# Kernel optimization log

Measured on AMD Instinct MI355X. Metric: run time of the kernel, lower is better.

The kernel has to match this reference:

```python
import jax, jax.numpy as jnp
import numpy as np

G = 384          # voxel grid extent per axis = (15.36*2)/0.08
HALF = G // 2
SZ = G
SYZ = G * G
SXYZ = G * G * G
VOX = 0.08       # layer voxel size (cfg voxel_size * coord_key)
CK = 2           # coord_key / tensor stride
K = 5            # grid conv kernel size -> 125 offsets
GN = 7           # grid_num -> 343 cells per ROI, pooling conv kernel
EPS = 1e-5


def _masked_bn(x, valid, gamma, beta):
    # training-mode batch norm over valid rows only
    v = valid[:, None].astype(x.dtype)
    n = jnp.maximum(v.sum(), 1.0)
    mean = (x * v).sum(0) / n
    var = (((x - mean) ** 2) * v).sum(0) / n
    return (x - mean) * jax.lax.rsqrt(var + EPS) * gamma + beta


def setup_inputs() -> dict:
    rng = np.random.default_rng(0)
    B, R, C = 4, 128, 128
    P = GN ** 3
    N = B * R * P           # 175616 grid points
    Nv = 200000             # active voxels in sp_tensor
    # unique sparse-tensor coordinates: sample linear codes, dedupe, decode
    codes = np.unique(rng.integers(0, B * SXYZ, size=3 * Nv))[:Nv]
    rng.shuffle(codes)
    sb = codes // SXYZ
    rem = codes % SXYZ
    vx, vy, vz = rem // SYZ, (rem % SYZ) // SZ, rem % SZ
    sp_coords = np.stack(
        [sb, (vx - HALF) * CK, (vy - HALF) * CK, (vz - HALF) * CK], 1
    ).astype(np.int32)
    # ROI grid points: dense (7,7,7) grids inside random boxes
    centers = rng.uniform(-12.0, 12.0, (B, R, 3)).astype(np.float32)
    sizes = rng.uniform(0.5, 3.0, (B, R, 3)).astype(np.float32)
    gi = np.stack(
        np.meshgrid(np.arange(GN), np.arange(GN), np.arange(GN), indexing='ij'), -1
    ).reshape(-1, 3).astype(np.float32)  # [343,3]
    pts = (centers[:, :, None, :] - sizes[:, :, None, :] / 2
           + (gi[None, None] + 0.5) / GN * sizes[:, :, None, :])  # [B,R,P,3]
    bcol = np.broadcast_to(np.arange(B, dtype=np.float32)[:, None, None, None], (B, R, P, 1))
    grid_points = np.concatenate([bcol, pts], -1).reshape(N, 4)
    k1, k2, k3 = jax.random.split(jax.random.key(0), 3)
    return {
        'sp_coords': jnp.asarray(sp_coords),
        'sp_feats': jax.random.normal(k1, (Nv, C), jnp.float32),
        'grid_points': jnp.asarray(grid_points),
        'W1': jax.random.normal(k2, (K ** 3, C, C), jnp.float32) * 0.01,
        'gamma1': jnp.ones((C,), jnp.float32),
        'beta1': jnp.zeros((C,), jnp.float32),
        'W2': jax.random.normal(k3, (P, C, C), jnp.float32) * 0.01,
        'gamma2': jnp.ones((C,), jnp.float32),
        'beta2': jnp.zeros((C,), jnp.float32),
    }


def reference(sp_coords, sp_feats, grid_points, W1, gamma1, beta1, W2, gamma2, beta2):
    N = grid_points.shape[0]
    C = sp_feats.shape[1]
    P = GN ** 3
    # --- voxelize grid points and merge coordinates (hash) ---
    vox = jnp.clip(jnp.floor(grid_points[:, 1:4] / VOX).astype(jnp.int32),
                   -(HALF - 1), HALF - 1)
    pos = vox + HALF
    bidx = grid_points[:, 0].astype(jnp.int32)
    mc = bidx * SXYZ + pos[:, 0] * SYZ + pos[:, 1] * SZ + pos[:, 2]
    unq, unq_inv = jnp.unique(mc, return_inverse=True, size=N, fill_value=-1)
    valid = unq >= 0
    u = jnp.maximum(unq, 0)
    qb = u // SXYZ
    qv = jnp.stack([u % SXYZ // SYZ, u % SYZ // SZ, u % SZ], 1)  # voxel idx [Nq,3]
    # --- hash table for sp_tensor coords (sorted linear codes) ---
    svi = sp_coords[:, 1:4] // CK + HALF
    scode = sp_coords[:, 0] * SXYZ + svi[:, 0] * SYZ + svi[:, 1] * SZ + svi[:, 2]
    order = jnp.argsort(scode)
    scodes = scode[order]
    sfeats = sp_feats[order]
    # --- Minkowski-style sparse conv: sum over 125 kernel offsets ---
    kr = jnp.arange(-(K // 2), K // 2 + 1)
    offs = jnp.stack(jnp.meshgrid(kr, kr, kr, indexing='ij'), -1).reshape(-1, 3)

    def body(acc, xs):
        off, Wk = xs
        tvi = qv + off
        inb = jnp.all((tvi >= 0) & (tvi < G), axis=1) & valid
        code = qb * SXYZ + tvi[:, 0] * SYZ + tvi[:, 1] * SZ + tvi[:, 2]
        p = jnp.clip(jnp.searchsorted(scodes, code), 0, scodes.shape[0] - 1)
        hit = (scodes[p] == code) & inb
        f = jnp.where(hit[:, None], sfeats[p], 0.0)
        return acc + f @ Wk, None

    acc, _ = jax.lax.scan(body, jnp.zeros((N, C), sp_feats.dtype), (offs, W1))
    x = jax.nn.elu(_masked_bn(acc, valid, gamma1, beta1))
    # gather back per grid point, then dense pooling conv over full 7^3 grid
    nf = x[unq_inv].reshape(-1, P, C)              # [num_rois, 343, C]
    pooled = jnp.einsum('bpc,pcd->bd', nf, W2)     # pooling conv at center
    mean = pooled.mean(0)
    var = pooled.var(0)
    return (pooled - mean) * jax.lax.rsqrt(var + EPS) * gamma2 + beta2
```

## Files before the change

kernel.cpp:

```cpp
#include <hip/hip_runtime.h>
#include <math.h>

#define GG     384
#define HALFG  192
#define SZc    384
#define SYZc   147456
#define SXYZc  56623104
#define CC     128
#define PP     343
#define KK     125
#define TBSLOTS (1 << 20)
#define TBMASK  (TBSLOTS - 1)
#define BMAXc   4
#define NCOL    (BMAXc * GG * GG)
#define TASLOTS (1 << 19)
#define TAMASK  (TASLOTS - 1)
#define CAPK   2048
#define CAPP   1024
#define EPSc   1e-5f
#define PAD    16

typedef unsigned long long u64;

__device__ __forceinline__ unsigned hash32(int code) {
    unsigned h = (unsigned)code;
    h ^= h >> 16; h *= 0x7feb352du;
    h ^= h >> 15; h *= 0x846ca68bu;
    h ^= h >> 16;
    return h;
}

__global__ void k_buildInsert(const float* __restrict__ gp, int2* tabA, int* slotA,
                              int* nq, int* ucode, int N, int nbA,
                              const int4* __restrict__ spc4, unsigned* tabB,
                              u64* colBM, int Nv) {
    if (blockIdx.x < nbA) {
        __shared__ int lcnt, lbase;
        if (threadIdx.x == 0) lcnt = 0;
        __syncthreads();
        int i = blockIdx.x * 256 + threadIdx.x;
        int myloc = -1; unsigned myh = 0; int code = 0;
        if (i < N) {
            float4 g = ((const float4*)gp)[i];
            int b = (int)g.x;
            int vx = (int)floorf(g.y / 0.08f); vx = min(max(vx, -(HALFG - 1)), HALFG - 1);
            int vy = (int)floorf(g.z / 0.08f); vy = min(max(vy, -(HALFG - 1)), HALFG - 1);
            int vz = (int)floorf(g.w / 0.08f); vz = min(max(vz, -(HALFG - 1)), HALFG - 1);
            code = b * SXYZc + (vx + HALFG) * SYZc + (vy + HALFG) * SZc + (vz + HALFG);
            unsigned h = hash32(code) & TAMASK;
            while (true) {
                int old = atomicCAS(&tabA[h].x, 0, code + 1);
                if (old == 0) { myloc = atomicAdd(&lcnt, 1); break; }
                if (old == code + 1) break;
                h = (h + 1) & TAMASK;
            }
            myh = h;
            slotA[i] = (int)h;
        }
        __syncthreads();
        if (threadIdx.x == 0 && lcnt > 0) lbase = atomicAdd(nq, lcnt);
        __syncthreads();
        if (myloc >= 0) {
            int uid = lbase + myloc;
            tabA[myh].y = uid;
            ucode[uid] = code;
        }
    } else {
        int i = (blockIdx.x - nbA) * 256 + threadIdx.x;
        if (i >= Nv) return;
        int4 s = spc4[i];
        int b = s.x;
        int x = (s.y >> 1) + HALFG;
        int y = (s.z >> 1) + HALFG;
        int z = (s.w >> 1) + HALFG;
        int code = b * SXYZc + x * SYZc + y * SZc + z;
        unsigned h = hash32(code);
        unsigned slot = h & TBMASK;
        unsigned val = ((h >> 18) << 18) | (unsigned)(i + 1);
        while (true) {
            unsigned old = atomicCAS(&tabB[slot], 0u, val);
            if (old == 0u) break;
            slot = (slot + 1) & TBMASK;
        }
        int col = (b * GG + x) * GG + y;
        atomicOr(&colBM[(size_t)col * 6 + (z >> 6)], 1ull << (z & 63));
    }
}

__global__ void k_probe(const int* __restrict__ ucode, const u64* __restrict__ colBM,
                        const unsigned* __restrict__ tabB, const int4* __restrict__ spc4,
                        int* hmark, int* cntk, int* bkUid, int* bkP,
                        const int* __restrict__ nqp, int N) {
    unsigned tid = blockIdx.x * 256u + threadIdx.x;
    if (tid >= (unsigned)N * 25u) return;
    unsigned uid = tid / 25u;
    if (uid >= (unsigned)(*nqp)) return;
    int c = (int)(tid - uid * 25u);
    unsigned code = (unsigned)ucode[uid];
    unsigned b = code / SXYZc; unsigned rem = code - b * SXYZc;
    int x = (int)(rem / SYZc); rem -= (unsigned)x * SYZc;
    int y = (int)(rem / SZc);
    int z = (int)(rem - (unsigned)y * SZc);
    int dx = c / 5, dy = c - dx * 5;
    int cx = x + dx - 2, cy = y + dy - 2;
    if ((unsigned)cx >= GG || (unsigned)cy >= GG) return;
    const u64* bm = colBM + (size_t)(((int)b * GG + cx) * GG + cy) * 6;
    int lo = max(z - 2, 0);
    int hi = min(z + 2, GG - 1);
    int width = hi - lo + 1;
    int i0 = lo >> 6, sh = lo & 63;
    u64 w = bm[i0] >> sh;
    if (sh + width > 64) w |= bm[i0 + 1] << (64 - sh);
    unsigned bits = (unsigned)(w & ((1ull << width) - 1ull));
    if (bits == 0) return;
    hmark[uid] = 1;
    int zbase = z - 2;
    while (bits) {
        int j = __builtin_ctz(bits);
        bits &= bits - 1;
        int tz = lo + j;
        int dz = tz - zbase;
        int k = c * 5 + dz;
        int tcode = (int)b * SXYZc + cx * SYZc + cy * SZc + tz;
        unsigned h = hash32(tcode);
        unsigned slot = h & TBMASK;
        unsigned tag = h >> 18;
        while (true) {
            unsigned v = tabB[slot];
            if (v == 0u) break;
            if ((v >> 18) == tag) {
                int row = (int)(v & 0x3FFFFu) - 1;
                int4 s = spc4[row];
                int rcode = s.x * SXYZc + ((s.y >> 1) + HALFG) * SYZc
                          + ((s.z >> 1) + HALFG) * SZc + ((s.w >> 1) + HALFG);
                if (rcode == tcode) {
                    int pos = atomicAdd(&cntk[k * PAD], 1);
                    if (pos < CAPK) { bkUid[k * CAPK + pos] = (int)uid; bkP[k * CAPK + pos] = row; }
                    break;
                }
            }
            slot = (slot + 1) & TBMASK;
        }
    }
}

__global__ void k_hitPairs(const int* __restrict__ hmark, int* hitList, int* nh,
                           float* acc, const int* __restrict__ nqp, int nbU,
                           const int* __restrict__ slotA, const int2* __restrict__ tabA,
                           int* pcnt, int* pairPack, int N) {
    if (blockIdx.x < nbU) {
        __shared__ int lcnt, lbase;
        if (threadIdx.x == 0) lcnt = 0;
        __syncthreads();
        int i = blockIdx.x * 256 + threadIdx.x;
        int myloc = -1;
        if (i < *nqp && hmark[i]) myloc = atomicAdd(&lcnt, 1);
        __syncthreads();
        if (threadIdx.x == 0 && lcnt > 0) lbase = atomicAdd(nh, lcnt);
        __syncthreads();
        if (myloc >= 0) {
            hitList[lbase + myloc] = i;
            float4* a4 = (float4*)(acc + (size_t)i * CC);
            float4 z4 = make_float4(0.f, 0.f, 0.f, 0.f);
            #pragma unroll
            for (int c = 0; c < CC / 4; c++) a4[c] = z4;
        }
    } else {
        int i = (blockIdx.x - nbU) * 256 + threadIdx.x;
        if (i >= N) return;
        int uid = tabA[slotA[i]].y;
        if (!hmark[uid]) return;
        int b = i / PP;
        int p = i - b * PP;
        int pos = atomicAdd(&pcnt[p * PAD], 1);
        if (pos < CAPP) pairPack[p * CAPP + pos] = (b << 18) | uid;
    }
}

__global__ __launch_bounds__(256) void k_conv(const float* __restrict__ spf,
        const float* __restrict__ W1, const int* __restrict__ cntk,
        const int* __restrict__ bkUid, const int* __restrict__ bkP, float* acc) {
    int k = blockIdx.x;
    int cob = blockIdx.y * 64;
    int t = threadIdx.x;
    int co = cob + (t & 63);
    int lane = t >> 6;
    int cnt = min(cntk[k * PAD], CAPK);
    __shared__ float fs[32][CC];
    __shared__ int hrS[32];
    const float* Wk = W1 + (size_t)k * CC * CC;
    for (int tile = blockIdx.z * 32; tile < cnt; tile += 32 * gridDim.z) {
        int nt = min(32, cnt - tile);
        if (t < nt) hrS[t] = bkUid[k * CAPK + tile + t];
        for (int e = t; e < 32 * CC; e += 256) {
            int r = e >> 7, cc = e & 127;
            fs[r][cc] = (r < nt) ? spf[(size_t)bkP[k * CAPK + tile + r] * CC + cc] : 0.f;
        }
        __syncthreads();
        float a[8] = {0.f, 0.f, 0.f, 0.f, 0.f, 0.f, 0.f, 0.f};
        for (int ci = 0; ci < CC; ci++) {
            float wv = Wk[(size_t)ci * CC + co];
            #pragma unroll
            for (int j = 0; j < 8; j++) a[j] += fs[lane * 8 + j][ci] * wv;
        }
        #pragma unroll
        for (int j = 0; j < 8; j++) {
            int r = lane * 8 + j;
            if (r < nt) atomicAdd(&acc[(size_t)hrS[r] * CC + co], a[j]);
        }
        __syncthreads();
    }
}

__global__ void k_stats(const float* __restrict__ acc, const int* __restrict__ hitList,
                        float* gsum, float* gsumsq, const int* __restrict__ nhp,
                        int* done, const float* __restrict__ g1, const float* __restrict__ b1,
                        float* scaleV, float* shiftV, float* c0v, const int* __restrict__ nqp) {
    int t = threadIdx.x; int c = t & 127; int half = t >> 7;
    int nh = *nhp;
    float s = 0.f, s2 = 0.f;
    for (int j = blockIdx.x * 2 + half; j < nh; j += gridDim.x * 2) {
        int r = hitList[j];
        float v = acc[(size_t)r * CC + c];
        s += v; s2 += v * v;
    }
    __shared__ float red[256];
    red[t] = s; __syncthreads();
    if (half == 0) atomicAdd(&gsum[c * PAD], s + red[t + 128]);
    __syncthreads();
    red[t] = s2; __syncthreads();
    if (half == 0) atomicAdd(&gsumsq[c * PAD], s2 + red[t + 128]);
    __syncthreads();
    __shared__ int lastS;
    if (t == 0) {
        __threadfence();
        lastS = (atomicAdd(done, 1) == gridDim.x - 1) ? 1 : 0;
    }
    __syncthreads();
    if (lastS && t < 128) {
        float n = (float)max(*nqp, 1);
        float sum  = atomicAdd(&gsum[t * PAD], 0.f);
        float sums = atomicAdd(&gsumsq[t * PAD], 0.f);
        float mean = sum / n;
        float var = sums / n - mean * mean;
        float rs = 1.0f / sqrtf(var + EPSc);
        float scale = rs * g1[t];
        float shift = b1[t] - mean * scale;
        float c0 = shift;
        c0 = c0 > 0.f ? c0 : expm1f(c0);
        scaleV[t] = scale; shiftV[t] = shift; c0v[t] = c0;
    }
}

__global__ __launch_bounds__(256) void k_pool(const float* __restrict__ acc,
        const float* __restrict__ W2, const int* __restrict__ pcnt,
        const int* __restrict__ pairPack,
        const float* __restrict__ scaleV, const float* __restrict__ shiftV,
        const float* __restrict__ c0v, float* pooled) {
    int p = blockIdx.x;
    int cob = blockIdx.y * 64;
    int t = threadIdx.x;
    int co = cob + (t & 63);
    int lane = t >> 6;
    int cnt = min(pcnt[p * PAD], CAPP);
    __shared__ float fs[32][CC];
    __shared__ int bS[32];
    __shared__ float scS[CC], shS[CC], c0S[CC];
    if (t < 128) { scS[t] = scaleV[t]; shS[t] = shiftV[t]; c0S[t] = c0v[t]; }
    __syncthreads();
    const float* Wp = W2 + (size_t)p * CC * CC;
    for (int tile = blockIdx.z * 32; tile < cnt; tile += 32 * gridDim.z) {
        int nt = min(32, cnt - tile);
        if (t < nt) bS[t] = pairPack[p * CAPP + tile + t] >> 18;
        for (int e = t; e < 32 * CC; e += 256) {
            int r = e >> 7, cc = e & 127;
            float v = 0.f;
            if (r < nt) {
                int uid = pairPack[p * CAPP + tile + r] & 0x3FFFF;
                float x = acc[(size_t)uid * CC + cc] * scS[cc] + shS[cc];
                x = x > 0.f ? x : expm1f(x);
                v = x - c0S[cc];
            }
            fs[r][cc] = v;
        }
        __syncthreads();
        float a[8] = {0.f, 0.f, 0.f, 0.f, 0.f, 0.f, 0.f, 0.f};
        for (int ci = 0; ci < CC; ci++) {
            float wv = Wp[(size_t)ci * CC + co];
            #pragma unroll
            for (int j = 0; j < 8; j++) a[j] += fs[lane * 8 + j][ci] * wv;
        }
        #pragma unroll
        for (int j = 0; j < 8; j++) {
            int r = lane * 8 + j;
            if (r < nt) atomicAdd(&pooled[(size_t)bS[r] * CC + co], a[j]);
        }
        __syncthreads();
    }
}

__global__ void k_bn2(const float* __restrict__ pooled, const float* __restrict__ g2,
                      const float* __restrict__ b2, float* out, int NB) {
    int d = blockIdx.x; int t = threadIdx.x;
    float s = 0.f;
    for (int b = t; b < NB; b += 64) s += pooled[(size_t)b * CC + d];
    for (int o = 32; o >= 1; o >>= 1) s += __shfl_xor(s, o, 64);
    float mean = s / (float)NB;
    float s2 = 0.f;
    for (int b = t; b < NB; b += 64) { float v = pooled[(size_t)b * CC + d] - mean; s2 += v * v; }
    for (int o = 32; o >= 1; o >>= 1) s2 += __shfl_xor(s2, o, 64);
    float rs = 1.0f / sqrtf(s2 / (float)NB + EPSc);
    float gg = g2[d], bb = b2[d];
    for (int b = t; b < NB; b += 64)
        out[(size_t)b * CC + d] = (pooled[(size_t)b * CC + d] - mean) * rs * gg + bb;
}

extern "C" void kernel_launch(void* const* d_in, const int* in_sizes, int n_in,
                              void* d_out, int out_size, void* d_ws, size_t ws_size,
                              hipStream_t stream) {
    (void)n_in; (void)out_size; (void)ws_size;
    const int*   spc = (const int*)d_in[0];
    const float* spf = (const float*)d_in[1];
    const float* gp  = (const float*)d_in[2];
    const float* W1  = (const float*)d_in[3];
    const float* g1  = (const float*)d_in[4];
    const float* b1  = (const float*)d_in[5];
    const float* W2  = (const float*)d_in[6];
    const float* g2  = (const float*)d_in[7];
    const float* b2  = (const float*)d_in[8];
    int Nv = in_sizes[0] / 4;
    int N  = in_sizes[2] / 4;
    int NB = N / PP;
    float* out = (float*)d_out;

    char* w = (char*)d_ws;
    char* zero0 = w;
    int* nq   = (int*)w;  int* nh = nq + 1;  int* done = nq + 2;  w += 64;
    unsigned* tabB = (unsigned*)w; w += (size_t)TBSLOTS * 4;
    int2*     tabA = (int2*)w;     w += (size_t)TASLOTS * 8;
    u64* colBM = (u64*)w;         w += (size_t)NCOL * 6 * 8;
    int* cntk = (int*)w;          w += 128 * PAD * 4;
    int* pcnt = (int*)w;          w += 344 * PAD * 4;
    float* gsum   = (float*)w;    w += 128 * PAD * 4;
    float* gsumsq = (float*)w;    w += 128 * PAD * 4;
    int* hmark    = (int*)w;      w += (size_t)N * 4;
    float* pooled = (float*)w;    w += (size_t)NB * CC * 4;
    size_t zbytes = (size_t)(w - zero0);
    float* scaleV = (float*)w;    w += 128 * 4;
    float* shiftV = (float*)w;    w += 128 * 4;
    float* c0v    = (float*)w;    w += 128 * 4;
    int* hitList = (int*)w;       w += (size_t)N * 4;
    int* ucode   = (int*)w;       w += (size_t)N * 4;
    int* slotA   = (int*)w;       w += (size_t)N * 4;
    int* bkUid   = (int*)w;       w += (size_t)KK * CAPK * 4;
    int* bkP     = (int*)w;       w += (size_t)KK * CAPK * 4;
    int* pairPack= (int*)w;       w += (size_t)PP * CAPP * 4;
    float* acc   = (float*)w;     w += (size_t)N * CC * 4;

    hipMemsetAsync(zero0, 0, zbytes, stream);

    int nbA = (N + 255) / 256;
    int nbB = (Nv + 255) / 256;
    k_buildInsert<<<nbA + nbB, 256, 0, stream>>>(gp, tabA, slotA, nq, ucode, N, nbA,
                                                 (const int4*)spc, tabB, colBM, Nv);
    long tot = (long)N * 25;
    k_probe  <<<(unsigned)((tot + 255) / 256), 256, 0, stream>>>(ucode, colBM, tabB,
                                                                 (const int4*)spc,
                                                                 hmark, cntk, bkUid, bkP, nq, N);
    int nbU = (N + 255) / 256;
    k_hitPairs<<<nbU + nbA, 256, 0, stream>>>(hmark, hitList, nh, acc, nq, nbU,
                                              slotA, tabA, pcnt, pairPack, N);
    k_conv   <<<dim3(KK, 2, 4), 256, 0, stream>>>(spf, W1, cntk, bkUid, bkP, acc);
    k_stats  <<<256, 256, 0, stream>>>(acc, hitList, gsum, gsumsq, nh, done,
                                       g1, b1, scaleV, shiftV, c0v, nq);
    k_pool   <<<dim3(PP, 2, 2), 256, 0, stream>>>(acc, W2, pcnt, pairPack,
                                                  scaleV, shiftV, c0v, pooled);
    k_bn2    <<<CC, 64, 0, stream>>>(pooled, g2, b2, out, NB);
}
```

Baseline: 350.2 us.

## Fuse whole pipeline into one cooperative persistent kernel with grid syncs

Replaces the memset and seven separate kernel launches with a single cooperative persistent kernel. Stages are separated by grid-wide barriers, and the in-kernel zeroing of the workspace replaces hipMemsetAsync. The goal is to remove per-launch overhead and the tail idle time between small dependent stages. The trade-offs are grid-stride loops in place of natural grid shapes, possibly lower occupancy for the heavy conv and pool stages, and the cost of the grid.sync barriers themselves.

```diff
diff --git a/kernel.cpp b/kernel.cpp
--- a/kernel.cpp
+++ b/kernel.cpp
@@ -1,5 +1,8 @@
 #include <hip/hip_runtime.h>
+#include <hip/hip_cooperative_groups.h>
 #include <math.h>
+
+namespace cg = cooperative_groups;
 
 #define GG     384
 #define HALFG  192
@@ -30,18 +33,44 @@
     return h;
 }
 
-__global__ void k_buildInsert(const float* __restrict__ gp, int2* tabA, int* slotA,
-                              int* nq, int* ucode, int N, int nbA,
-                              const int4* __restrict__ spc4, unsigned* tabB,
-                              u64* colBM, int Nv) {
-    if (blockIdx.x < nbA) {
-        __shared__ int lcnt, lbase;
-        if (threadIdx.x == 0) lcnt = 0;
-        __syncthreads();
-        int i = blockIdx.x * 256 + threadIdx.x;
+struct Prm {
+    const float* gp; const int4* spc4; const float* spf;
+    const float* W1; const float* g1; const float* b1;
+    const float* W2; const float* g2; const float* b2;
+    float* out;
+    int2* tabA; unsigned* tabB; u64* colBM;
+    int* slotA; int* ucode; int* nq; int* nh;
+    int* hmark; int* hitList; int* cntk; int* pcnt;
+    int* bkUid; int* bkP; int* pairPack;
+    float* gsum; float* gsumsq; float* acc; float* pooled;
+    float4* zero0; size_t z16; int N; int Nv; int NB;
+};
+
+__global__ __launch_bounds__(256, 4) void k_fused(Prm p) {
+    cg::grid_group grid = cg::this_grid();
+    const int nb = (int)gridDim.x;
+    const int bid = blockIdx.x, t = threadIdx.x;
+
+    __shared__ float fs[32][CC];
+    __shared__ int idxS[32];
+    __shared__ float scS[CC], shS[CC], c0S[CC];
+    __shared__ float red[256];
+    __shared__ int lcnt, lbase;
+
+    {
+        float4 z4 = make_float4(0.f, 0.f, 0.f, 0.f);
+        for (size_t e = (size_t)bid * 256 + t; e < p.z16; e += (size_t)nb * 256)
+            p.zero0[e] = z4;
+    }
+    grid.sync();
+
+    for (int base = bid * 256; base < p.N; base += nb * 256) {
+        if (t == 0) lcnt = 0;
+        __syncthreads();
+        int i = base + t;
         int myloc = -1; unsigned myh = 0; int code = 0;
-        if (i < N) {
-            float4 g = ((const float4*)gp)[i];
+        if (i < p.N) {
+            float4 g = ((const float4*)p.gp)[i];
             int b = (int)g.x;
             int vx = (int)floorf(g.y / 0.08f); vx = min(max(vx, -(HALFG - 1)), HALFG - 1);
             int vy = (int)floorf(g.z / 0.08f); vy = min(max(vy, -(HALFG - 1)), HALFG - 1);
@@ -49,26 +78,26 @@
             code = b * SXYZc + (vx + HALFG) * SYZc + (vy + HALFG) * SZc + (vz + HALFG);
             unsigned h = hash32(code) & TAMASK;
             while (true) {
-                int old = atomicCAS(&tabA[h].x, 0, code + 1);
+                int old = atomicCAS(&p.tabA[h].x, 0, code + 1);
                 if (old == 0) { myloc = atomicAdd(&lcnt, 1); break; }
                 if (old == code + 1) break;
                 h = (h + 1) & TAMASK;
             }
             myh = h;
-            slotA[i] = (int)h;
-        }
-        __syncthreads();
-        if (threadIdx.x == 0 && lcnt > 0) lbase = atomicAdd(nq, lcnt);
+            p.slotA[i] = (int)h;
+        }
+        __syncthreads();
+        if (t == 0 && lcnt > 0) lbase = atomicAdd(p.nq, lcnt);
         __syncthreads();
         if (myloc >= 0) {
             int uid = lbase + myloc;
-            tabA[myh].y = uid;
-            ucode[uid] = code;
-        }
-    } else {
-        int i = (blockIdx.x - nbA) * 256 + threadIdx.x;
-        if (i >= Nv) return;
-        int4 s = spc4[i];
+            p.tabA[myh].y = uid;
+            p.ucode[uid] = code;
+        }
+        __syncthreads();
+    }
+    for (int i = bid * 256 + t; i < p.Nv; i += nb * 256) {
+        int4 s = p.spc4[i];
         int b = s.x;
         int x = (s.y >> 1) + HALFG;
         int y = (s.z >> 1) + HALFG;
@@ -78,302 +107,271 @@
         unsigned slot = h & TBMASK;
         unsigned val = ((h >> 18) << 18) | (unsigned)(i + 1);
         while (true) {
-            unsigned old = atomicCAS(&tabB[slot], 0u, val);
+            unsigned old = atomicCAS(&p.tabB[slot], 0u, val);
             if (old == 0u) break;
             slot = (slot + 1) & TBMASK;
         }
         int col = (b * GG + x) * GG + y;
-        atomicOr(&colBM[(size_t)col * 6 + (z >> 6)], 1ull << (z & 63));
-    }
-}
-
-__global__ void k_probe(const int* __restrict__ ucode, const u64* __restrict__ colBM,
-                        const unsigned* __restrict__ tabB, const int4* __restrict__ spc4,
-                        int* hmark, int* cntk, int* bkUid, int* bkP,
-                        const int* __restrict__ nqp, int N) {
-    unsigned tid = blockIdx.x * 256u + threadIdx.x;
-    if (tid >= (unsigned)N * 25u) return;
-    unsigned uid = tid / 25u;
-    if (uid >= (unsigned)(*nqp)) return;
-    int c = (int)(tid - uid * 25u);
-    unsigned code = (unsigned)ucode[uid];
-    unsigned b = code / SXYZc; unsigned rem = code - b * SXYZc;
-    int x = (int)(rem / SYZc); rem -= (unsigned)x * SYZc;
-    int y = (int)(rem / SZc);
-    int z = (int)(rem - (unsigned)y * SZc);
-    int dx = c / 5, dy = c - dx * 5;
-    int cx = x + dx - 2, cy = y + dy - 2;
-    if ((unsigned)cx >= GG || (unsigned)cy >= GG) return;
-    const u64* bm = colBM + (size_t)(((int)b * GG + cx) * GG + cy) * 6;
-    int lo = max(z - 2, 0);
-    int hi = min(z + 2, GG - 1);
-    int width = hi - lo + 1;
-    int i0 = lo >> 6, sh = lo & 63;
-    u64 w = bm[i0] >> sh;
-    if (sh + width > 64) w |= bm[i0 + 1] << (64 - sh);
-    unsigned bits = (unsigned)(w & ((1ull << width) - 1ull));
-    if (bits == 0) return;
-    hmark[uid] = 1;
-    int zbase = z - 2;
-    while (bits) {
-        int j = __builtin_ctz(bits);
-        bits &= bits - 1;
-        int tz = lo + j;
-        int dz = tz - zbase;
-        int k = c * 5 + dz;
-        int tcode = (int)b * SXYZc + cx * SYZc + cy * SZc + tz;
-        unsigned h = hash32(tcode);
-        unsigned slot = h & TBMASK;
-        unsigned tag = h >> 18;
-        while (true) {
-            unsigned v = tabB[slot];
-            if (v == 0u) break;
-            if ((v >> 18) == tag) {
-                int row = (int)(v & 0x3FFFFu) - 1;
-                int4 s = spc4[row];
-                int rcode = s.x * SXYZc + ((s.y >> 1) + HALFG) * SYZc
-                          + ((s.z >> 1) + HALFG) * SZc + ((s.w >> 1) + HALFG);
-                if (rcode == tcode) {
-                    int pos = atomicAdd(&cntk[k * PAD], 1);
-                    if (pos < CAPK) { bkUid[k * CAPK + pos] = (int)uid; bkP[k * CAPK + pos] = row; }
-                    break;
+        atomicOr(&p.colBM[(size_t)col * 6 + (z >> 6)], 1ull << (z & 63));
+    }
+    grid.sync();
+
+    if (t == 0) idxS[0] = *p.nq;
+    __syncthreads();
+    const int nqv = idxS[0];
+    __syncthreads();
+    {
+        long tot = (long)nqv * 25;
+        for (long e0 = (long)bid * 256 + t; e0 < tot; e0 += (long)nb * 256) {
+            unsigned uid = (unsigned)(e0 / 25);
+            int c = (int)(e0 - (long)uid * 25);
+            unsigned code = (unsigned)p.ucode[uid];
+            unsigned b = code / SXYZc; unsigned rem = code - b * SXYZc;
+            int x = (int)(rem / SYZc); rem -= (unsigned)x * SYZc;
+            int y = (int)(rem / SZc);
+            int z = (int)(rem - (unsigned)y * SZc);
+            int dx = c / 5, dy = c - dx * 5;
+            int cx = x + dx - 2, cy = y + dy - 2;
+            if ((unsigned)cx >= GG || (unsigned)cy >= GG) continue;
+            const u64* bm = p.colBM + (size_t)(((int)b * GG + cx) * GG + cy) * 6;
+            int lo = max(z - 2, 0);
+            int hi = min(z + 2, GG - 1);
+            int width = hi - lo + 1;
+            int i0 = lo >> 6, sh = lo & 63;
+            u64 w = bm[i0] >> sh;
+            if (sh + width > 64) w |= bm[i0 + 1] << (64 - sh);
+            unsigned bits = (unsigned)(w & ((1ull << width) - 1ull));
+            if (bits == 0) continue;
+            p.hmark[uid] = 1;
+            int zbase = z - 2;
+            while (bits) {
+                int j = __builtin_ctz(bits);
+                bits &= bits - 1;
+                int tz = lo + j;
+                int dz = tz - zbase;
+                int k = c * 5 + dz;
+                int tcode = (int)b * SXYZc + cx * SYZc + cy * SZc + tz;
+                unsigned h = hash32(tcode);
+                unsigned slot = h & TBMASK;
+                unsigned tag = h >> 18;
+                while (true) {
+                    unsigned v = p.tabB[slot];
+                    if (v == 0u) break;
+                    if ((v >> 18) == tag) {
+                        int row = (int)(v & 0x3FFFFu) - 1;
+                        int4 s = p.spc4[row];
+                        int rcode = s.x * SXYZc + ((s.y >> 1) + HALFG) * SYZc
+                                  + ((s.z >> 1) + HALFG) * SZc + ((s.w >> 1) + HALFG);
+                        if (rcode == tcode) {
+                            int pos = atomicAdd(&p.cntk[k * PAD], 1);
+                            if (pos < CAPK) { p.bkUid[k * CAPK + pos] = (int)uid; p.bkP[k * CAPK + pos] = row; }
+                            break;
+                        }
+                    }
+                    slot = (slot + 1) & TBMASK;
                 }
             }
-            slot = (slot + 1) & TBMASK;
-        }
-    }
-}
-
-__global__ void k_hitPairs(const int* __restrict__ hmark, int* hitList, int* nh,
-                           float* acc, const int* __restrict__ nqp, int nbU,
-                           const int* __restrict__ slotA, const int2* __restrict__ tabA,
-                           int* pcnt, int* pairPack, int N) {
-    if (blockIdx.x < nbU) {
-        __shared__ int lcnt, lbase;
-        if (threadIdx.x == 0) lcnt = 0;
-        __syncthreads();
-        int i = blockIdx.x * 256 + threadIdx.x;
+        }
+    }
+    grid.sync();
+
+    for (int base = bid * 256; base < nqv; base += nb * 256) {
+        if (t == 0) lcnt = 0;
+        __syncthreads();
+        int i = base + t;
         int myloc = -1;
-        if (i < *nqp && hmark[i]) myloc = atomicAdd(&lcnt, 1);
-        __syncthreads();
-        if (threadIdx.x == 0 && lcnt > 0) lbase = atomicAdd(nh, lcnt);
+        if (i < nqv && p.hmark[i]) myloc = atomicAdd(&lcnt, 1);
+        __syncthreads();
+        if (t == 0 && lcnt > 0) lbase = atomicAdd(p.nh, lcnt);
         __syncthreads();
         if (myloc >= 0) {
-            hitList[lbase + myloc] = i;
-            float4* a4 = (float4*)(acc + (size_t)i * CC);
+            p.hitList[lbase + myloc] = i;
+            float4* a4 = (float4*)(p.acc + (size_t)i * CC);
             float4 z4 = make_float4(0.f, 0.f, 0.f, 0.f);
             #pragma unroll
             for (int c = 0; c < CC / 4; c++) a4[c] = z4;
         }
-    } else {
-        int i = (blockIdx.x - nbU) * 256 + threadIdx.x;
-        if (i >= N) return;
-        int uid = tabA[slotA[i]].y;
-        if (!hmark[uid]) return;
+        __syncthreads();
+    }
+    for (int i = bid * 256 + t; i < p.N; i += nb * 256) {
+        int uid = p.tabA[p.slotA[i]].y;
+        if (!p.hmark[uid]) continue;
         int b = i / PP;
-        int p = i - b * PP;
-        int pos = atomicAdd(&pcnt[p * PAD], 1);
-        if (pos < CAPP) pairPack[p * CAPP + pos] = (b << 18) | uid;
-    }
-}
-
-__global__ __launch_bounds__(256) void k_conv(const float* __restrict__ spf,
-        const float* __restrict__ W1, const int* __restrict__ cntk,
-        const int* __restrict__ bkUid, const int* __restrict__ bkP, float* acc) {
-    int k = blockIdx.x;
-    int cob = blockIdx.y * 64;
-    int t = threadIdx.x;
-    int co = cob + (t & 63);
-    int lane = t >> 6;
-    int cnt = min(cntk[k * PAD], CAPK);
-    __shared__ float fs[32][CC];
-    __shared__ int hrS[32];
-    const float* Wk = W1 + (size_t)k * CC * CC;
-    for (int tile = blockIdx.z * 32; tile < cnt; tile += 32 * gridDim.z) {
-        int nt = min(32, cnt - tile);
-        if (t < nt) hrS[t] = bkUid[k * CAPK + tile + t];
-        for (int e = t; e < 32 * CC; e += 256) {
-            int r = e >> 7, cc = e & 127;
-            fs[r][cc] = (r < nt) ? spf[(size_t)bkP[k * CAPK + tile + r] * CC + cc] : 0.f;
-        }
-        __syncthreads();
-        float a[8] = {0.f, 0.f, 0.f, 0.f, 0.f, 0.f, 0.f, 0.f};
-        for (int ci = 0; ci < CC; ci++) {
-            float wv = Wk[(size_t)ci * CC + co];
+        int pp = i - b * PP;
+        int pos = atomicAdd(&p.pcnt[pp * PAD], 1);
+        if (pos < CAPP) p.pairPack[pp * CAPP + pos] = (b << 18) | uid;
+    }
+    grid.sync();
+
+    for (int v = bid; v < KK * 8; v += nb) {
+        int k = v >> 3;
+        int cob = ((v >> 2) & 1) * 64;
+        int zz = v & 3;
+        int co = cob + (t & 63);
+        int lane = t >> 6;
+        int cnt = min(p.cntk[k * PAD], CAPK);
+        const float* Wk = p.W1 + (size_t)k * CC * CC;
+        for (int tile = zz * 32; tile < cnt; tile += 32 * 4) {
+            int nt = min(32, cnt - tile);
+            if (t < nt) idxS[t] = p.bkUid[k * CAPK + tile + t];
+            for (int e = t; e < 32 * CC; e += 256) {
+                int r = e >> 7, cc = e & 127;
+                fs[r][cc] = (r < nt) ? p.spf[(size_t)p.bkP[k * CAPK + tile + r] * CC + cc] : 0.f;
+            }
+            __syncthreads();
+            float a[8] = {0.f, 0.f, 0.f, 0.f, 0.f, 0.f, 0.f, 0.f};
+            for (int ci = 0; ci < CC; ci++) {
+                float wv = Wk[(size_t)ci * CC + co];
+                #pragma unroll
+                for (int j = 0; j < 8; j++) a[j] += fs[lane * 8 + j][ci] * wv;
+            }
             #pragma unroll
-            for (int j = 0; j < 8; j++) a[j] += fs[lane * 8 + j][ci] * wv;
-        }
-        #pragma unroll
-        for (int j = 0; j < 8; j++) {
-            int r = lane * 8 + j;
-            if (r < nt) atomicAdd(&acc[(size_t)hrS[r] * CC + co], a[j]);
-        }
-        __syncthreads();
-    }
-}
-
-__global__ void k_stats(const float* __restrict__ acc, const int* __restrict__ hitList,
-                        float* gsum, float* gsumsq, const int* __restrict__ nhp,
-                        int* done, const float* __restrict__ g1, const float* __restrict__ b1,
-                        float* scaleV, float* shiftV, float* c0v, const int* __restrict__ nqp) {
-    int t = threadIdx.x; int c = t & 127; int half = t >> 7;
-    int nh = *nhp;
-    float s = 0.f, s2 = 0.f;
-    for (int j = blockIdx.x * 2 + half; j < nh; j += gridDim.x * 2) {
-        int r = hitList[j];
-        float v = acc[(size_t)r * CC + c];
-        s += v; s2 += v * v;
-    }
-    __shared__ float red[256];
-    red[t] = s; __syncthreads();
-    if (half == 0) atomicAdd(&gsum[c * PAD], s + red[t + 128]);
-    __syncthreads();
-    red[t] = s2; __syncthreads();
-    if (half == 0) atomicAdd(&gsumsq[c * PAD], s2 + red[t + 128]);
-    __syncthreads();
-    __shared__ int lastS;
-    if (t == 0) {
-        __threadfence();
-        lastS = (atomicAdd(done, 1) == gridDim.x - 1) ? 1 : 0;
-    }
-    __syncthreads();
-    if (lastS && t < 128) {
-        float n = (float)max(*nqp, 1);
-        float sum  = atomicAdd(&gsum[t * PAD], 0.f);
-        float sums = atomicAdd(&gsumsq[t * PAD], 0.f);
+            for (int j = 0; j < 8; j++) {
+                int r = lane * 8 + j;
+                if (r < nt) atomicAdd(&p.acc[(size_t)idxS[r] * CC + co], a[j]);
+            }
+            __syncthreads();
+        }
+    }
+    grid.sync();
+
+    if (t == 0) idxS[0] = *p.nh;
+    __syncthreads();
+    const int nhv = idxS[0];
+    __syncthreads();
+    {
+        int c = t & 127, half = t >> 7;
+        float s = 0.f, s2 = 0.f;
+        for (int j = bid * 2 + half; j < nhv; j += nb * 2) {
+            int r = p.hitList[j];
+            float v = p.acc[(size_t)r * CC + c];
+            s += v; s2 += v * v;
+        }
+        red[t] = s; __syncthreads();
+        if (half == 0) atomicAdd(&p.gsum[c * PAD], s + red[t + 128]);
+        __syncthreads();
+        red[t] = s2; __syncthreads();
+        if (half == 0) atomicAdd(&p.gsumsq[c * PAD], s2 + red[t + 128]);
+    }
+    grid.sync();
+
+    if (t < 128) {
+        float n = (float)max(nqv, 1);
+        float sum  = p.gsum[t * PAD];
+        float sums = p.gsumsq[t * PAD];
         float mean = sum / n;
         float var = sums / n - mean * mean;
         float rs = 1.0f / sqrtf(var + EPSc);
-        float scale = rs * g1[t];
-        float shift = b1[t] - mean * scale;
-        float c0 = shift;
-        c0 = c0 > 0.f ? c0 : expm1f(c0);
-        scaleV[t] = scale; shiftV[t] = shift; c0v[t] = c0;
-    }
-}
-
-__global__ __launch_bounds__(256) void k_pool(const float* __restrict__ acc,
-        const float* __restrict__ W2, const int* __restrict__ pcnt,
-        const int* __restrict__ pairPack,
-        const float* __restrict__ scaleV, const float* __restrict__ shiftV,
-        const float* __restrict__ c0v, float* pooled) {
-    int p = blockIdx.x;
-    int cob = blockIdx.y * 64;
-    int t = threadIdx.x;
-    int co = cob + (t & 63);
-    int lane = t >> 6;
-    int cnt = min(pcnt[p * PAD], CAPP);
-    __shared__ float fs[32][CC];
-    __shared__ int bS[32];
-    __shared__ float scS[CC], shS[CC], c0S[CC];
-    if (t < 128) { scS[t] = scaleV[t]; shS[t] = shiftV[t]; c0S[t] = c0v[t]; }
-    __syncthreads();
-    const float* Wp = W2 + (size_t)p * CC * CC;
-    for (int tile = blockIdx.z * 32; tile < cnt; tile += 32 * gridDim.z) {
-        int nt = min(32, cnt - tile);
-        if (t < nt) bS[t] = pairPack[p * CAPP + tile + t] >> 18;
-        for (int e = t; e < 32 * CC; e += 256) {
-            int r = e >> 7, cc = e & 127;
-            float v = 0.f;
-            if (r < nt) {
-                int uid = pairPack[p * CAPP + tile + r] & 0x3FFFF;
-                float x = acc[(size_t)uid * CC + cc] * scS[cc] + shS[cc];
-                x = x > 0.f ? x : expm1f(x);
-                v = x - c0S[cc];
-            }
-            fs[r][cc] = v;
-        }
-        __syncthreads();
-        float a[8] = {0.f, 0.f, 0.f, 0.f, 0.f, 0.f, 0.f, 0.f};
-        for (int ci = 0; ci < CC; ci++) {
-            float wv = Wp[(size_t)ci * CC + co];
+        float scale = rs * p.g1[t];
+        float shift = p.b1[t] - mean * scale;
+        float c0 = shift > 0.f ? shift : expm1f(shift);
+        scS[t] = scale; shS[t] = shift; c0S[t] = c0;
+    }
+    __syncthreads();
+    for (int v = bid; v < PP * 4; v += nb) {
+        int pp = v >> 2;
+        int cob = ((v >> 1) & 1) * 64;
+        int zz = v & 1;
+        int co = cob + (t & 63);
+        int lane = t >> 6;
+        int cnt = min(p.pcnt[pp * PAD], CAPP);
+        const float* Wp = p.W2 + (size_t)pp * CC * CC;
+        for (int tile = zz * 32; tile < cnt; tile += 32 * 2) {
+            int nt = min(32, cnt - tile);
+            if (t < nt) idxS[t] = p.pairPack[pp * CAPP + tile + t] >> 18;
+            for (int e = t; e < 32 * CC; e += 256) {
+                int r = e >> 7, cc = e & 127;
+                float val = 0.f;
+                if (r < nt) {
+                    int uid = p.pairPack[pp * CAPP + tile + r] & 0x3FFFF;
+                    float x = p.acc[(size_t)uid * CC + cc] * scS[cc] + shS[cc];
+                    x = x > 0.f ? x : expm1f(x);
+                    val = x - c0S[cc];
+                }
+                fs[r][cc] = val;
+            }
+            __syncthreads();
+            float a[8] = {0.f, 0.f, 0.f, 0.f, 0.f, 0.f, 0.f, 0.f};
+            for (int ci = 0; ci < CC; ci++) {
+                float wv = Wp[(size_t)ci * CC + co];
+                #pragma unroll
+                for (int j = 0; j < 8; j++) a[j] += fs[lane * 8 + j][ci] * wv;
+            }
             #pragma unroll
-            for (int j = 0; j < 8; j++) a[j] += fs[lane * 8 + j][ci] * wv;
-        }
-        #pragma unroll
-        for (int j = 0; j < 8; j++) {
-            int r = lane * 8 + j;
-            if (r < nt) atomicAdd(&pooled[(size_t)bS[r] * CC + co], a[j]);
-        }
-        __syncthreads();
-    }
-}
-
-__global__ void k_bn2(const float* __restrict__ pooled, const float* __restrict__ g2,
-                      const float* __restrict__ b2, float* out, int NB) {
-    int d = blockIdx.x; int t = threadIdx.x;
-    float s = 0.f;
-    for (int b = t; b < NB; b += 64) s += pooled[(size_t)b * CC + d];
-    for (int o = 32; o >= 1; o >>= 1) s += __shfl_xor(s, o, 64);
-    float mean = s / (float)NB;
-    float s2 = 0.f;
-    for (int b = t; b < NB; b += 64) { float v = pooled[(size_t)b * CC + d] - mean; s2 += v * v; }
-    for (int o = 32; o >= 1; o >>= 1) s2 += __shfl_xor(s2, o, 64);
-    float rs = 1.0f / sqrtf(s2 / (float)NB + EPSc);
-    float gg = g2[d], bb = b2[d];
-    for (int b = t; b < NB; b += 64)
-        out[(size_t)b * CC + d] = (pooled[(size_t)b * CC + d] - mean) * rs * gg + bb;
+            for (int j = 0; j < 8; j++) {
+                int r = lane * 8 + j;
+                if (r < nt) atomicAdd(&p.pooled[(size_t)idxS[r] * CC + co], a[j]);
+            }
+            __syncthreads();
+        }
+    }
+    grid.sync();
+
+    if (bid < CC / 4) {
+        int d = bid * 4 + (t >> 6);
+        int ln = t & 63;
+        float s = 0.f;
+        for (int b = ln; b < p.NB; b += 64) s += p.pooled[(size_t)b * CC + d];
+        for (int o = 32; o >= 1; o >>= 1) s += __shfl_xor(s, o, 64);
+        float mean = s / (float)p.NB;
+        float s2 = 0.f;
+        for (int b = ln; b < p.NB; b += 64) { float v = p.pooled[(size_t)b * CC + d] - mean; s2 += v * v; }
+        for (int o = 32; o >= 1; o >>= 1) s2 += __shfl_xor(s2, o, 64);
+        float rs = 1.0f / sqrtf(s2 / (float)p.NB + EPSc);
+        float gg = p.g2[d], bb = p.b2[d];
+        for (int b = ln; b < p.NB; b += 64)
+            p.out[(size_t)b * CC + d] = (p.pooled[(size_t)b * CC + d] - mean) * rs * gg + bb;
+    }
 }
 
 extern "C" void kernel_launch(void* const* d_in, const int* in_sizes, int n_in,
                               void* d_out, int out_size, void* d_ws, size_t ws_size,
                               hipStream_t stream) {
     (void)n_in; (void)out_size; (void)ws_size;
-    const int*   spc = (const int*)d_in[0];
-    const float* spf = (const float*)d_in[1];
-    const float* gp  = (const float*)d_in[2];
-    const float* W1  = (const float*)d_in[3];
-    const float* g1  = (const float*)d_in[4];
-    const float* b1  = (const float*)d_in[5];
-    const float* W2  = (const float*)d_in[6];
-    const float* g2  = (const float*)d_in[7];
-    const float* b2  = (const float*)d_in[8];
+    Prm p;
+    p.gp   = (const float*)d_in[2];
+    p.spc4 = (const int4*)d_in[0];
+    p.spf  = (const float*)d_in[1];
+    p.W1   = (const float*)d_in[3];
+    p.g1   = (const float*)d_in[4];
+    p.b1   = (const float*)d_in[5];
+    p.W2   = (const float*)d_in[6];
+    p.g2   = (const float*)d_in[7];
+    p.b2   = (const float*)d_in[8];
+    p.out  = (float*)d_out;
     int Nv = in_sizes[0] / 4;
     int N  = in_sizes[2] / 4;
-    int NB = N / PP;
-    float* out = (float*)d_out;
+    p.N = N; p.Nv = Nv; p.NB = N / PP;
 
     char* w = (char*)d_ws;
     char* zero0 = w;
-    int* nq   = (int*)w;  int* nh = nq + 1;  int* done = nq + 2;  w += 64;
-    unsigned* tabB = (unsigned*)w; w += (size_t)TBSLOTS * 4;
-    int2*     tabA = (int2*)w;     w += (size_t)TASLOTS * 8;
-    u64* colBM = (u64*)w;         w += (size_t)NCOL * 6 * 8;
-    int* cntk = (int*)w;          w += 128 * PAD * 4;
-    int* pcnt = (int*)w;          w += 344 * PAD * 4;
-    float* gsum   = (float*)w;    w += 128 * PAD * 4;
-    float* gsumsq = (float*)w;    w += 128 * PAD * 4;
-    int* hmark    = (int*)w;      w += (size_t)N * 4;
-    float* pooled = (float*)w;    w += (size_t)NB * CC * 4;
+    p.nq = (int*)w;  p.nh = p.nq + 1;  w += 64;
+    p.tabB = (unsigned*)w; w += (size_t)TBSLOTS * 4;
+    p.tabA = (int2*)w;     w += (size_t)TASLOTS * 8;
+    p.colBM = (u64*)w;     w += (size_t)NCOL * 6 * 8;
+    p.cntk = (int*)w;      w += 128 * PAD * 4;
+    p.pcnt = (int*)w;      w += 344 * PAD * 4;
+    p.gsum   = (float*)w;  w += 128 * PAD * 4;
+    p.gsumsq = (float*)w;  w += 128 * PAD * 4;
+    p.hmark  = (int*)w;    w += (size_t)N * 4;
+    p.pooled = (float*)w;  w += (size_t)p.NB * CC * 4;
     size_t zbytes = (size_t)(w - zero0);
-    float* scaleV = (float*)w;    w += 128 * 4;
-    float* shiftV = (float*)w;    w += 128 * 4;
-    float* c0v    = (float*)w;    w += 128 * 4;
-    int* hitList = (int*)w;       w += (size_t)N * 4;
-    int* ucode   = (int*)w;       w += (size_t)N * 4;
-    int* slotA   = (int*)w;       w += (size_t)N * 4;
-    int* bkUid   = (int*)w;       w += (size_t)KK * CAPK * 4;
-    int* bkP     = (int*)w;       w += (size_t)KK * CAPK * 4;
-    int* pairPack= (int*)w;       w += (size_t)PP * CAPP * 4;
-    float* acc   = (float*)w;     w += (size_t)N * CC * 4;
-
-    hipMemsetAsync(zero0, 0, zbytes, stream);
-
-    int nbA = (N + 255) / 256;
-    int nbB = (Nv + 255) / 256;
-    k_buildInsert<<<nbA + nbB, 256, 0, stream>>>(gp, tabA, slotA, nq, ucode, N, nbA,
-                                                 (const int4*)spc, tabB, colBM, Nv);
-    long tot = (long)N * 25;
-    k_probe  <<<(unsigned)((tot + 255) / 256), 256, 0, stream>>>(ucode, colBM, tabB,
-                                                                 (const int4*)spc,
-                                                                 hmark, cntk, bkUid, bkP, nq, N);
-    int nbU = (N + 255) / 256;
-    k_hitPairs<<<nbU + nbA, 256, 0, stream>>>(hmark, hitList, nh, acc, nq, nbU,
-                                              slotA, tabA, pcnt, pairPack, N);
-    k_conv   <<<dim3(KK, 2, 4), 256, 0, stream>>>(spf, W1, cntk, bkUid, bkP, acc);
-    k_stats  <<<256, 256, 0, stream>>>(acc, hitList, gsum, gsumsq, nh, done,
-                                       g1, b1, scaleV, shiftV, c0v, nq);
-    k_pool   <<<dim3(PP, 2, 2), 256, 0, stream>>>(acc, W2, pcnt, pairPack,
-                                                  scaleV, shiftV, c0v, pooled);
-    k_bn2    <<<CC, 64, 0, stream>>>(pooled, g2, b2, out, NB);
+    p.zero0 = (float4*)zero0;
+    p.z16 = zbytes / 16;
+    p.hitList = (int*)w;   w += (size_t)N * 4;
+    p.ucode   = (int*)w;   w += (size_t)N * 4;
+    p.slotA   = (int*)w;   w += (size_t)N * 4;
+    p.bkUid   = (int*)w;   w += (size_t)KK * CAPK * 4;
+    p.bkP     = (int*)w;   w += (size_t)KK * CAPK * 4;
+    p.pairPack= (int*)w;   w += (size_t)PP * CAPP * 4;
+    p.acc     = (float*)w; w += (size_t)N * CC * 4;
+
+    int nbpc = 0;
+    hipOccupancyMaxActiveBlocksPerMultiprocessor(&nbpc, k_fused, 256, 0);
+    if (nbpc < 1) nbpc = 1;
+    long grid = (long)nbpc * 256;
+    if (grid > 2048) grid = 2048;
+    void* args[] = { (void*)&p };
+    hipLaunchCooperativeKernel((const void*)k_fused, dim3((unsigned)grid), dim3(256),
+                               args, 0, stream);
 }
```

After: 806.6 us. 2.3x slower.
